# Kernel optimization log

Measured on AMD Instinct MI355X. Metric: run time of the kernel, lower is better.

Reference implementation:

```python
import jax, jax.numpy as jnp
import numpy as np

NUM_GRAPHS = 512
NODES_PER_GRAPH = 200  # == N_rois
EDGES_PER_GRAPH = 3200  # avg degree 16
N_ROIS = 200
HIDDEN = 64
OUT = 2


def setup_inputs() -> dict:
    key = jax.random.key(0)
    ks = jax.random.split(key, 7)
    N = NUM_GRAPHS * NODES_PER_GRAPH
    E = NUM_GRAPHS * EDGES_PER_GRAPH
    x = jax.random.normal(ks[0], (N, N_ROIS), dtype=jnp.float32)
    # edges sampled within each graph's node block
    base = jnp.repeat(jnp.arange(NUM_GRAPHS, dtype=jnp.int64) * NODES_PER_GRAPH, EDGES_PER_GRAPH)
    local = jax.random.randint(ks[1], (2, E), 0, NODES_PER_GRAPH, dtype=jnp.int64)
    edge_index = local + base[None, :]
    batch = jnp.arange(N, dtype=jnp.int64) // NODES_PER_GRAPH
    conv_w = jax.random.normal(ks[2], (N_ROIS, HIDDEN), dtype=jnp.float32) * 0.1
    conv_b = jax.random.normal(ks[3], (HIDDEN,), dtype=jnp.float32) * 0.1
    lin_w = jax.random.normal(ks[4], (HIDDEN, OUT), dtype=jnp.float32) * 0.1
    lin_b = jax.random.normal(ks[5], (OUT,), dtype=jnp.float32) * 0.1
    return {"x": x, "edge_index": edge_index, "batch": batch,
            "conv_w": conv_w, "conv_b": conv_b, "lin_w": lin_w, "lin_b": lin_b}


def reference(x, edge_index, batch, conv_w, conv_b, lin_w, lin_b):
    N = x.shape[0]
    # GCNConv: linear transform first (N_rois -> hidden), then normalized aggregation
    h = x @ conv_w  # [N, H]
    loops = jnp.arange(N, dtype=edge_index.dtype)
    src = jnp.concatenate([edge_index[0], loops])  # add self-loops (PyG default)
    dst = jnp.concatenate([edge_index[1], loops])
    deg = jax.ops.segment_sum(jnp.ones_like(dst, dtype=h.dtype), dst, num_segments=N)
    dinv = jnp.where(deg > 0, jax.lax.rsqrt(deg), jnp.zeros_like(deg))
    norm = dinv[src] * dinv[dst]  # D^-1/2 (A+I) D^-1/2 edge weights
    agg = jax.ops.segment_sum(h[src] * norm[:, None], dst, num_segments=N) + conv_b
    hr = jax.nn.relu(agg)
    x_pool = jax.ops.segment_max(hr, batch, num_segments=NUM_GRAPHS)  # [G, H]
    out = x_pool @ lin_w + lin_b  # [G, OUT]
    return out, x_pool
```

## Files before the change

kernel.cpp:

```cpp
#include <hip/hip_runtime.h>

#define NUM_GRAPHS 512
#define NPG 200
#define EPG 3200
#define NROIS 200
#define HID 64
#define OUTC 2
#define APITCH 232
#define HPITCH 232
#define XPITCH 72
#define WIMG_ELEMS (7 * 4 * 2 * 64 * 8)
#define WS_NEEDED ((size_t)WIMG_ELEMS * 2)

typedef short v8s __attribute__((ext_vector_type(8)));
typedef float v4f __attribute__((ext_vector_type(4)));

__device__ __forceinline__ unsigned bf16_rne(float f) {
  unsigned u = __float_as_uint(f);
  return (u + 0x7fffu + ((u >> 16) & 1u)) >> 16;
}

__global__ void prep_wimg(const float* __restrict__ cw, unsigned short* __restrict__ wimg) {
  int idx = blockIdx.x * 256 + threadIdx.x;
  if (idx >= WIMG_ELEMS) return;
  int i    = idx & 7;
  int lane = (idx >> 3) & 63;
  int hl   = (idx >> 9) & 1;
  int nt   = (idx >> 10) & 3;
  int kt   = idx >> 12;
  int k  = kt * 32 + (lane >> 4) * 8 + i;
  int ch = nt * 16 + (lane & 15);
  float f = (k < NROIS) ? cw[k * HID + ch] : 0.f;
  unsigned hi = bf16_rne(f);
  float lo = f - __uint_as_float(hi << 16);
  wimg[idx] = hl ? (unsigned short)(__float_as_uint(lo) >> 16) : (unsigned short)hi;
}

struct __align__(16) SmemU {
  union {
    struct {
      unsigned short xhi[NPG * XPITCH];
      unsigned short xlo[NPG * XPITCH];
    } g1;
    struct {
      unsigned char adj[208 * APITCH];
      unsigned short hpTl[HID * HPITCH];
    } g2;
  } u;
  float dinv[NPG];
  int cnt[NPG];
  int pool[HID];
};

__device__ __forceinline__ void stage_x(SmemU& s, const float* __restrict__ x,
                                        int base, int tk, int tid) {
  const int c0 = tk * 64;
  #pragma unroll
  for (int r = 0; r < 7; ++r) {
    int idx = tid + r * 512;
    if (idx < NPG * 16) {
      int node = idx >> 4;
      int f4 = idx & 15;
      int col = c0 + f4 * 4;
      float ff[4];
      if (col + 4 <= NROIS) {
        const float4 v = *(const float4*)(x + (size_t)(base + node) * NROIS + col);
        ff[0] = v.x; ff[1] = v.y; ff[2] = v.z; ff[3] = v.w;
      } else {
        #pragma unroll
        for (int e = 0; e < 4; ++e)
          ff[e] = (col + e < NROIS) ? x[(size_t)(base + node) * NROIS + col + e] : 0.f;
      }
      unsigned hh[4], ll[4];
      #pragma unroll
      for (int e = 0; e < 4; ++e) {
        unsigned uu = __float_as_uint(ff[e]);
        hh[e] = uu >> 16;
        float lo = ff[e] - __uint_as_float(hh[e] << 16);
        ll[e] = __float_as_uint(lo) >> 16;
      }
      uint2 ph = {hh[0] | (hh[1] << 16), hh[2] | (hh[3] << 16)};
      uint2 pl = {ll[0] | (ll[1] << 16), ll[2] | (ll[3] << 16)};
      *(uint2*)&s.u.g1.xhi[node * XPITCH + f4 * 4] = ph;
      *(uint2*)&s.u.g1.xlo[node * XPITCH + f4 * 4] = pl;
    }
  }
}

__global__ __launch_bounds__(512, 4)
void gcn_fused2(const float* __restrict__ x,
                const int* __restrict__ ei,
                const unsigned short* __restrict__ wimg,
                const float* __restrict__ cb,
                const float* __restrict__ lw,
                const float* __restrict__ lb,
                float* __restrict__ out,
                int Etot) {
  __shared__ SmemU s;
  const int g = blockIdx.x;
  const int tid = threadIdx.x;
  const int base = g * NPG;
  const int ebase = g * EPG;
  const int lane = tid & 63;
  const int w = __builtin_amdgcn_readfirstlane(tid >> 6);
  const int ml = tid & 15;
  const int q  = (tid >> 4) & 3;

  if (tid < NPG) s.cnt[tid] = 0;
  if (tid < HID) s.pool[tid] = 0;
  __syncthreads();

  int esrc[7], edst[7];
  #pragma unroll
  for (int r = 0; r < 7; ++r) {
    int e = tid + r * 512;
    esrc[r] = -1; edst[r] = 0;
    if (e < EPG) {
      esrc[r] = ei[ebase + e] - base;
      edst[r] = ei[Etot + ebase + e] - base;
      atomicAdd(&s.cnt[edst[r]], 1);
    }
  }
  stage_x(s, x, base, 0, tid);
  __syncthreads();

  if (tid < NPG) s.dinv[tid] = rsqrtf((float)(s.cnt[tid] + 1));

  int mts[2];
  mts[0] = w;
  mts[1] = (w < 5) ? 8 + w : -1;

  v4f acc[2][4];
  #pragma unroll
  for (int a = 0; a < 2; ++a)
    #pragma unroll
    for (int b = 0; b < 4; ++b)
      acc[a][b] = (v4f){0.f, 0.f, 0.f, 0.f};

  for (int tk = 0; tk < 4; ++tk) {
    #pragma unroll
    for (int half = 0; half < 2; ++half) {
      const int kt = tk * 2 + half;
      if (kt < 7) {
        const int koff = half * 32 + q * 8;
        v8s whi[4], wlo[4];
        #pragma unroll
        for (int nt = 0; nt < 4; ++nt) {
          const unsigned short* pw = wimg + (size_t)(((kt * 4 + nt) * 2) * 64 + lane) * 8;
          whi[nt] = *(const v8s*)pw;
          wlo[nt] = *(const v8s*)(pw + 64 * 8);
        }
        #pragma unroll
        for (int mi = 0; mi < 2; ++mi) {
          if (mts[mi] >= 0) {
            const int node = mts[mi] * 16 + ml;
            const int nrd = (node < NPG) ? node : 0;
            const v8s xh = *(const v8s*)&s.u.g1.xhi[nrd * XPITCH + koff];
            const v8s xl = *(const v8s*)&s.u.g1.xlo[nrd * XPITCH + koff];
            #pragma unroll
            for (int nt = 0; nt < 4; ++nt) {
              acc[mi][nt] = __builtin_amdgcn_mfma_f32_16x16x32_bf16(whi[nt], xl, acc[mi][nt], 0, 0, 0);
              acc[mi][nt] = __builtin_amdgcn_mfma_f32_16x16x32_bf16(wlo[nt], xh, acc[mi][nt], 0, 0, 0);
              acc[mi][nt] = __builtin_amdgcn_mfma_f32_16x16x32_bf16(whi[nt], xh, acc[mi][nt], 0, 0, 0);
            }
          }
        }
      }
    }
    __syncthreads();
    if (tk < 3) {
      stage_x(s, x, base, tk + 1, tid);
      __syncthreads();
    }
  }

  {
    uint4* z = (uint4*)&s.u;
    const uint4 z4 = {0u, 0u, 0u, 0u};
    #pragma unroll
    for (int i = 0; i < 10; ++i) {
      int idx = tid + i * 512;
      if (idx < (208 * APITCH + HID * HPITCH * 2) / 16) z[idx] = z4;
    }
  }
  __syncthreads();

  #pragma unroll
  for (int mi = 0; mi < 2; ++mi) {
    if (mts[mi] >= 0) {
      const int node = mts[mi] * 16 + ml;
      if (node < NPG) {
        const float dv = s.dinv[node];
        #pragma unroll
        for (int nt = 0; nt < 4; ++nt) {
          #pragma unroll
          for (int r = 0; r < 4; ++r) {
            const int ch = nt * 16 + q * 4 + r;
            s.u.g2.hpTl[ch * HPITCH + node] = (unsigned short)bf16_rne(dv * acc[mi][nt][r]);
          }
        }
      }
    }
  }
  {
    unsigned* adjW = (unsigned*)s.u.g2.adj;
    #pragma unroll
    for (int r = 0; r < 7; ++r) {
      if (esrc[r] >= 0) {
        int idx = edst[r] * APITCH + esrc[r];
        atomicAdd(&adjW[idx >> 2], 1u << ((idx & 3) * 8));
      }
    }
    if (tid < NPG) {
      int idx = tid * APITCH + tid;
      atomicAdd(&adjW[idx >> 2], 1u << ((idx & 3) * 8));
    }
  }
  __syncthreads();

  {
    v4f acc2[2][4];
    #pragma unroll
    for (int a = 0; a < 2; ++a)
      #pragma unroll
      for (int b = 0; b < 4; ++b)
        acc2[a][b] = (v4f){0.f, 0.f, 0.f, 0.f};

    for (int kt = 0; kt < 7; ++kt) {
      const int k0 = kt * 32 + q * 8;

      v8s bf[4];
      #pragma unroll
      for (int nt = 0; nt < 4; ++nt)
        bf[nt] = *(const v8s*)&s.u.g2.hpTl[(nt * 16 + ml) * HPITCH + k0];

      #pragma unroll
      for (int mi = 0; mi < 2; ++mi) {
        if (mts[mi] >= 0) {
          const int row = mts[mi] * 16 + ml;
          const uint2 dd = *(const uint2*)&s.u.g2.adj[row * APITCH + k0];
          v8s af;
          #pragma unroll
          for (int i = 0; i < 4; ++i) {
            af[i]     = (short)(__float_as_uint((float)((dd.x >> (8 * i)) & 0xffu)) >> 16);
            af[i + 4] = (short)(__float_as_uint((float)((dd.y >> (8 * i)) & 0xffu)) >> 16);
          }
          #pragma unroll
          for (int nt = 0; nt < 4; ++nt)
            acc2[mi][nt] = __builtin_amdgcn_mfma_f32_16x16x32_bf16(af, bf[nt], acc2[mi][nt], 0, 0, 0);
        }
      }
    }

    float cbv[4];
    #pragma unroll
    for (int nt = 0; nt < 4; ++nt) cbv[nt] = cb[nt * 16 + ml];
    float mx[4] = {0.f, 0.f, 0.f, 0.f};
    #pragma unroll
    for (int mi = 0; mi < 2; ++mi) {
      if (mts[mi] >= 0) {
        #pragma unroll
        for (int r = 0; r < 4; ++r) {
          const int row = mts[mi] * 16 + q * 4 + r;
          if (row < NPG) {
            const float dv = s.dinv[row];
            #pragma unroll
            for (int nt = 0; nt < 4; ++nt) {
              float v = fmaxf(fmaf(dv, acc2[mi][nt][r], cbv[nt]), 0.f);
              mx[nt] = fmaxf(mx[nt], v);
            }
          }
        }
      }
    }
    #pragma unroll
    for (int nt = 0; nt < 4; ++nt) {
      mx[nt] = fmaxf(mx[nt], __shfl_xor(mx[nt], 16));
      mx[nt] = fmaxf(mx[nt], __shfl_xor(mx[nt], 32));
    }
    if (q == 0 && (lane >> 5) == 0) {
      #pragma unroll
      for (int nt = 0; nt < 4; ++nt)
        atomicMax(&s.pool[nt * 16 + ml], __float_as_int(mx[nt]));
    }
  }
  __syncthreads();

  if (tid < HID) {
    const float xp = __int_as_float(s.pool[tid]);
    out[NUM_GRAPHS * OUTC + g * HID + tid] = xp;
    float p0 = xp * lw[tid * 2 + 0];
    float p1 = xp * lw[tid * 2 + 1];
    #pragma unroll
    for (int off = 32; off > 0; off >>= 1) {
      p0 += __shfl_down(p0, off);
      p1 += __shfl_down(p1, off);
    }
    if (tid == 0) {
      out[g * OUTC + 0] = p0 + lb[0];
      out[g * OUTC + 1] = p1 + lb[1];
    }
  }
}

struct __align__(16) SmemF {
  unsigned char adj[208 * APITCH];
  unsigned short hpT[HID * HPITCH];
  float dinv[NPG];
  int cnt[NPG];
  int pool[HID];
};

__global__ __launch_bounds__(512, 4)
void gcn_fused_fb(const float* __restrict__ x,
                  const int* __restrict__ ei,
                  const float* __restrict__ cw,
                  const float* __restrict__ cb,
                  const float* __restrict__ lw,
                  const float* __restrict__ lb,
                  float* __restrict__ out,
                  int Etot) {
  __shared__ SmemF s;
  const int g = blockIdx.x;
  const int tid = threadIdx.x;
  const int base = g * NPG;
  const int ebase = g * EPG;
  const int lane = tid & 63;
  const int w = __builtin_amdgcn_readfirstlane(tid >> 6);
  const int ml = tid & 15;
  const int q  = (tid >> 4) & 3;

  {
    uint4* z = (uint4*)&s;
    const uint4 z4 = {0u, 0u, 0u, 0u};
    #pragma unroll
    for (int i = 0; i < 10; ++i) {
      int idx = tid + i * 512;
      if (idx < (208 * APITCH + HID * HPITCH * 2) / 16) z[idx] = z4;
    }
    if (tid < NPG) s.cnt[tid] = 0;
    if (tid < HID) s.pool[tid] = 0;
  }
  __syncthreads();

  int esrc[7], edst[7];
  #pragma unroll
  for (int r = 0; r < 7; ++r) {
    int e = tid + r * 512;
    esrc[r] = -1; edst[r] = 0;
    if (e < EPG) {
      esrc[r] = ei[ebase + e] - base;
      edst[r] = ei[Etot + ebase + e] - base;
      atomicAdd(&s.cnt[edst[r]], 1);
    }
  }
  __syncthreads();

  if (tid < NPG) s.dinv[tid] = rsqrtf((float)(s.cnt[tid] + 1));

  {
    unsigned* adjW = (unsigned*)s.adj;
    #pragma unroll
    for (int r = 0; r < 7; ++r) {
      if (esrc[r] >= 0) {
        int idx = edst[r] * APITCH + esrc[r];
        atomicAdd(&adjW[idx >> 2], 1u << ((idx & 3) * 8));
      }
    }
    if (tid < NPG) {
      int idx = tid * APITCH + tid;
      atomicAdd(&adjW[idx >> 2], 1u << ((idx & 3) * 8));
    }
  }
  __syncthreads();

  {
    int mts[2];
    mts[0] = w;
    mts[1] = (w < 5) ? 8 + w : -1;
    v4f acc[2][4];
    #pragma unroll
    for (int a = 0; a < 2; ++a)
      #pragma unroll
      for (int b = 0; b < 4; ++b)
        acc[a][b] = (v4f){0.f, 0.f, 0.f, 0.f};

    for (int kt = 0; kt < 7; ++kt) {
      const int k0 = kt * 32 + q * 8;
      const bool kok = (k0 < NROIS);
      v8s bhi[4], blo[4];
      #pragma unroll
      for (int nt = 0; nt < 4; ++nt) {
        #pragma unroll
        for (int i = 0; i < 8; ++i) {
          float f = kok ? cw[(k0 + i) * HID + nt * 16 + ml] : 0.f;
          unsigned hb = bf16_rne(f);
          float lo = f - __uint_as_float(hb << 16);
          bhi[nt][i] = (short)hb;
          blo[nt][i] = (short)(__float_as_uint(lo) >> 16);
        }
      }
      #pragma unroll
      for (int mi = 0; mi < 2; ++mi) {
        if (mts[mi] >= 0) {
          const int row = mts[mi] * 16 + ml;
          v8s ahi, alo;
          if (kok && row < NPG) {
            const float* px = x + (size_t)(base + row) * NROIS + k0;
            const float4 f0 = *(const float4*)px;
            const float4 f1 = *(const float4*)(px + 4);
            const float ff[8] = {f0.x, f0.y, f0.z, f0.w, f1.x, f1.y, f1.z, f1.w};
            #pragma unroll
            for (int i = 0; i < 8; ++i) {
              unsigned u = __float_as_uint(ff[i]);
              unsigned hb = u >> 16;
              float lo = ff[i] - __uint_as_float(hb << 16);
              ahi[i] = (short)hb;
              alo[i] = (short)(__float_as_uint(lo) >> 16);
            }
          } else {
            #pragma unroll
            for (int i = 0; i < 8; ++i) { ahi[i] = 0; alo[i] = 0; }
          }
          #pragma unroll
          for (int nt = 0; nt < 4; ++nt) {
            acc[mi][nt] = __builtin_amdgcn_mfma_f32_16x16x32_bf16(ahi, blo[nt], acc[mi][nt], 0, 0, 0);
            acc[mi][nt] = __builtin_amdgcn_mfma_f32_16x16x32_bf16(alo, bhi[nt], acc[mi][nt], 0, 0, 0);
            acc[mi][nt] = __builtin_amdgcn_mfma_f32_16x16x32_bf16(ahi, bhi[nt], acc[mi][nt], 0, 0, 0);
          }
        }
      }
    }
    #pragma unroll
    for (int mi = 0; mi < 2; ++mi) {
      if (mts[mi] >= 0) {
        #pragma unroll
        for (int r = 0; r < 4; ++r) {
          const int row = mts[mi] * 16 + q * 4 + r;
          if (row < NPG) {
            const float dv = s.dinv[row];
            #pragma unroll
            for (int nt = 0; nt < 4; ++nt)
              s.hpT[(nt * 16 + ml) * HPITCH + row] =
                  (unsigned short)bf16_rne(dv * acc[mi][nt][r]);
          }
        }
      }
    }
  }
  __syncthreads();

  {
    int mts[2];
    mts[0] = w;
    mts[1] = (w < 5) ? 8 + w : -1;
    v4f acc2[2][4];
    #pragma unroll
    for (int a = 0; a < 2; ++a)
      #pragma unroll
      for (int b = 0; b < 4; ++b)
        acc2[a][b] = (v4f){0.f, 0.f, 0.f, 0.f};

    for (int kt = 0; kt < 7; ++kt) {
      const int k0 = kt * 32 + q * 8;
      v8s bf[4];
      #pragma unroll
      for (int nt = 0; nt < 4; ++nt)
        bf[nt] = *(const v8s*)&s.hpT[(nt * 16 + ml) * HPITCH + k0];
      #pragma unroll
      for (int mi = 0; mi < 2; ++mi) {
        if (mts[mi] >= 0) {
          const int row = mts[mi] * 16 + ml;
          const uint2 dd = *(const uint2*)&s.adj[row * APITCH + k0];
          v8s af;
          #pragma unroll
          for (int i = 0; i < 4; ++i) {
            af[i]     = (short)(__float_as_uint((float)((dd.x >> (8 * i)) & 0xffu)) >> 16);
            af[i + 4] = (short)(__float_as_uint((float)((dd.y >> (8 * i)) & 0xffu)) >> 16);
          }
          #pragma unroll
          for (int nt = 0; nt < 4; ++nt)
            acc2[mi][nt] = __builtin_amdgcn_mfma_f32_16x16x32_bf16(af, bf[nt], acc2[mi][nt], 0, 0, 0);
        }
      }
    }

    float cbv[4];
    #pragma unroll
    for (int nt = 0; nt < 4; ++nt) cbv[nt] = cb[nt * 16 + ml];
    float mx[4] = {0.f, 0.f, 0.f, 0.f};
    #pragma unroll
    for (int mi = 0; mi < 2; ++mi) {
      if (mts[mi] >= 0) {
        #pragma unroll
        for (int r = 0; r < 4; ++r) {
          const int row = mts[mi] * 16 + q * 4 + r;
          if (row < NPG) {
            const float dv = s.dinv[row];
            #pragma unroll
            for (int nt = 0; nt < 4; ++nt) {
              float v = fmaxf(fmaf(dv, acc2[mi][nt][r], cbv[nt]), 0.f);
              mx[nt] = fmaxf(mx[nt], v);
            }
          }
        }
      }
    }
    #pragma unroll
    for (int nt = 0; nt < 4; ++nt) {
      mx[nt] = fmaxf(mx[nt], __shfl_xor(mx[nt], 16));
      mx[nt] = fmaxf(mx[nt], __shfl_xor(mx[nt], 32));
    }
    if (q == 0 && (lane >> 5) == 0) {
      #pragma unroll
      for (int nt = 0; nt < 4; ++nt)
        atomicMax(&s.pool[nt * 16 + ml], __float_as_int(mx[nt]));
    }
  }
  __syncthreads();

  if (tid < HID) {
    const float xp = __int_as_float(s.pool[tid]);
    out[NUM_GRAPHS * OUTC + g * HID + tid] = xp;
    float p0 = xp * lw[tid * 2 + 0];
    float p1 = xp * lw[tid * 2 + 1];
    #pragma unroll
    for (int off = 32; off > 0; off >>= 1) {
      p0 += __shfl_down(p0, off);
      p1 += __shfl_down(p1, off);
    }
    if (tid == 0) {
      out[g * OUTC + 0] = p0 + lb[0];
      out[g * OUTC + 1] = p1 + lb[1];
    }
  }
}

extern "C" void kernel_launch(void* const* d_in, const int* in_sizes, int n_in,
                              void* d_out, int out_size, void* d_ws, size_t ws_size,
                              hipStream_t stream) {
  const float* x  = (const float*)d_in[0];
  const int*   ei = (const int*)d_in[1];
  const float* cw = (const float*)d_in[3];
  const float* cb = (const float*)d_in[4];
  const float* lw = (const float*)d_in[5];
  const float* lb = (const float*)d_in[6];
  const int Etot = in_sizes[1] / 2;

  if (ws_size >= WS_NEEDED) {
    unsigned short* wimg = (unsigned short*)d_ws;
    prep_wimg<<<(WIMG_ELEMS + 255) / 256, 256, 0, stream>>>(cw, wimg);
    gcn_fused2<<<NUM_GRAPHS, 512, 0, stream>>>(x, ei, wimg, cb, lw, lb,
                                               (float*)d_out, Etot);
  } else {
    gcn_fused_fb<<<NUM_GRAPHS, 512, 0, stream>>>(x, ei, cw, cb, lw, lb,
                                                 (float*)d_out, Etot);
  }
}
```

Before: 154.5 us.

## Register-prefetch x tiles, build adjacency early, derive degree from adjacency rows

The x staging is split into a global load into registers and a later shared-memory write. The next 32-column tile is now prefetched while MFMAs run on the current one, so global latency overlaps compute. The adjacency matrix moves out of the union and is built at kernel start, which removes the separate count atomics. Degrees are then computed by summing byte counts in each adjacency row. This adds more barriers (seven k-steps instead of four), more registers for the prefetch, and a different shared-memory footprint that may affect occupancy.

```diff
diff --git a/kernel.cpp b/kernel.cpp
--- a/kernel.cpp
+++ b/kernel.cpp
@@ -8,7 +8,7 @@
 #define OUTC 2
 #define APITCH 232
 #define HPITCH 232
-#define XPITCH 72
+#define XPITCH 40
 #define WIMG_ELEMS (7 * 4 * 2 * 64 * 8)
 #define WS_NEEDED ((size_t)WIMG_ELEMS * 2)
 
@@ -37,40 +37,37 @@
 }
 
 struct __align__(16) SmemU {
+  unsigned char adj[208 * APITCH];
   union {
-    struct {
-      unsigned short xhi[NPG * XPITCH];
-      unsigned short xlo[NPG * XPITCH];
-    } g1;
-    struct {
-      unsigned char adj[208 * APITCH];
-      unsigned short hpTl[HID * HPITCH];
-    } g2;
+    struct { unsigned short xhi[NPG * XPITCH];
+             unsigned short xlo[NPG * XPITCH]; } g1;
+    unsigned short hpTl[HID * HPITCH];
   } u;
   float dinv[NPG];
-  int cnt[NPG];
   int pool[HID];
 };
 
-__device__ __forceinline__ void stage_x(SmemU& s, const float* __restrict__ x,
-                                        int base, int tk, int tid) {
-  const int c0 = tk * 64;
+__device__ __forceinline__ void xload(float4* xf, const float* __restrict__ x,
+                                      int base, int c0, int tid) {
   #pragma unroll
-  for (int r = 0; r < 7; ++r) {
+  for (int r = 0; r < 4; ++r) {
     int idx = tid + r * 512;
-    if (idx < NPG * 16) {
-      int node = idx >> 4;
-      int f4 = idx & 15;
-      int col = c0 + f4 * 4;
-      float ff[4];
-      if (col + 4 <= NROIS) {
-        const float4 v = *(const float4*)(x + (size_t)(base + node) * NROIS + col);
-        ff[0] = v.x; ff[1] = v.y; ff[2] = v.z; ff[3] = v.w;
-      } else {
-        #pragma unroll
-        for (int e = 0; e < 4; ++e)
-          ff[e] = (col + e < NROIS) ? x[(size_t)(base + node) * NROIS + col + e] : 0.f;
-      }
+    int node = idx >> 3, f4 = idx & 7;
+    int col = c0 + f4 * 4;
+    if (idx < 1600 && col + 4 <= NROIS)
+      xf[r] = *(const float4*)(x + (size_t)(base + node) * NROIS + col);
+    else
+      xf[r] = make_float4(0.f, 0.f, 0.f, 0.f);
+  }
+}
+
+__device__ __forceinline__ void xwrite(SmemU& s, const float4* xf, int tid) {
+  #pragma unroll
+  for (int r = 0; r < 4; ++r) {
+    int idx = tid + r * 512;
+    if (idx < 1600) {
+      int node = idx >> 3, f4 = idx & 7;
+      const float ff[4] = {xf[r].x, xf[r].y, xf[r].z, xf[r].w};
       unsigned hh[4], ll[4];
       #pragma unroll
       for (int e = 0; e < 4; ++e) {
@@ -88,7 +85,7 @@
 }
 
 __global__ __launch_bounds__(512, 4)
-void gcn_fused2(const float* __restrict__ x,
+void gcn_fused3(const float* __restrict__ x,
                 const int* __restrict__ ei,
                 const unsigned short* __restrict__ wimg,
                 const float* __restrict__ cb,
@@ -106,10 +103,8 @@
   const int ml = tid & 15;
   const int q  = (tid >> 4) & 3;
 
-  if (tid < NPG) s.cnt[tid] = 0;
-  if (tid < HID) s.pool[tid] = 0;
-  __syncthreads();
-
+  float4 xf[4];
+  xload(xf, x, base, 0, tid);
   int esrc[7], edst[7];
   #pragma unroll
   for (int r = 0; r < 7; ++r) {
@@ -118,13 +113,36 @@
     if (e < EPG) {
       esrc[r] = ei[ebase + e] - base;
       edst[r] = ei[Etot + ebase + e] - base;
-      atomicAdd(&s.cnt[edst[r]], 1);
-    }
-  }
-  stage_x(s, x, base, 0, tid);
-  __syncthreads();
-
-  if (tid < NPG) s.dinv[tid] = rsqrtf((float)(s.cnt[tid] + 1));
+    }
+  }
+  {
+    uint4* z = (uint4*)s.adj;
+    const uint4 z4 = {0u, 0u, 0u, 0u};
+    #pragma unroll
+    for (int i = 0; i < 6; ++i) {
+      int idx = tid + i * 512;
+      if (idx < (208 * APITCH) / 16) z[idx] = z4;
+    }
+    if (tid < HID) s.pool[tid] = 0;
+  }
+  __syncthreads();
+
+  {
+    unsigned* adjW = (unsigned*)s.adj;
+    #pragma unroll
+    for (int r = 0; r < 7; ++r) {
+      if (esrc[r] >= 0) {
+        int idx = edst[r] * APITCH + esrc[r];
+        atomicAdd(&adjW[idx >> 2], 1u << ((idx & 3) * 8));
+      }
+    }
+    if (tid < NPG) {
+      int idx = tid * APITCH + tid;
+      atomicAdd(&adjW[idx >> 2], 1u << ((idx & 3) * 8));
+    }
+  }
+  xwrite(s, xf, tid);
+  __syncthreads();
 
   int mts[2];
   mts[0] = w;
@@ -137,51 +155,50 @@
     for (int b = 0; b < 4; ++b)
       acc[a][b] = (v4f){0.f, 0.f, 0.f, 0.f};
 
-  for (int tk = 0; tk < 4; ++tk) {
-    #pragma unroll
-    for (int half = 0; half < 2; ++half) {
-      const int kt = tk * 2 + half;
-      if (kt < 7) {
-        const int koff = half * 32 + q * 8;
-        v8s whi[4], wlo[4];
+  for (int kt = 0; kt < 7; ++kt) {
+    float4 xfn[4];
+    if (kt < 6) xload(xfn, x, base, (kt + 1) * 32, tid);
+
+    v8s whi[4], wlo[4];
+    #pragma unroll
+    for (int nt = 0; nt < 4; ++nt) {
+      const unsigned short* pw = wimg + (size_t)(((kt * 4 + nt) * 2) * 64 + lane) * 8;
+      whi[nt] = *(const v8s*)pw;
+      wlo[nt] = *(const v8s*)(pw + 64 * 8);
+    }
+    #pragma unroll
+    for (int mi = 0; mi < 2; ++mi) {
+      if (mts[mi] >= 0) {
+        const int node = mts[mi] * 16 + ml;
+        const int nrd = (node < NPG) ? node : 0;
+        const v8s xh = *(const v8s*)&s.u.g1.xhi[nrd * XPITCH + q * 8];
+        const v8s xl = *(const v8s*)&s.u.g1.xlo[nrd * XPITCH + q * 8];
         #pragma unroll
         for (int nt = 0; nt < 4; ++nt) {
-          const unsigned short* pw = wimg + (size_t)(((kt * 4 + nt) * 2) * 64 + lane) * 8;
-          whi[nt] = *(const v8s*)pw;
-          wlo[nt] = *(const v8s*)(pw + 64 * 8);
-        }
-        #pragma unroll
-        for (int mi = 0; mi < 2; ++mi) {
-          if (mts[mi] >= 0) {
-            const int node = mts[mi] * 16 + ml;
-            const int nrd = (node < NPG) ? node : 0;
-            const v8s xh = *(const v8s*)&s.u.g1.xhi[nrd * XPITCH + koff];
-            const v8s xl = *(const v8s*)&s.u.g1.xlo[nrd * XPITCH + koff];
-            #pragma unroll
-            for (int nt = 0; nt < 4; ++nt) {
-              acc[mi][nt] = __builtin_amdgcn_mfma_f32_16x16x32_bf16(whi[nt], xl, acc[mi][nt], 0, 0, 0);
-              acc[mi][nt] = __builtin_amdgcn_mfma_f32_16x16x32_bf16(wlo[nt], xh, acc[mi][nt], 0, 0, 0);
-              acc[mi][nt] = __builtin_amdgcn_mfma_f32_16x16x32_bf16(whi[nt], xh, acc[mi][nt], 0, 0, 0);
-            }
-          }
+          acc[mi][nt] = __builtin_amdgcn_mfma_f32_16x16x32_bf16(whi[nt], xl, acc[mi][nt], 0, 0, 0);
+          acc[mi][nt] = __builtin_amdgcn_mfma_f32_16x16x32_bf16(wlo[nt], xh, acc[mi][nt], 0, 0, 0);
+          acc[mi][nt] = __builtin_amdgcn_mfma_f32_16x16x32_bf16(whi[nt], xh, acc[mi][nt], 0, 0, 0);
         }
       }
     }
     __syncthreads();
-    if (tk < 3) {
-      stage_x(s, x, base, tk + 1, tid);
+    if (kt < 6) {
+      xwrite(s, xfn, tid);
       __syncthreads();
     }
   }
 
-  {
-    uint4* z = (uint4*)&s.u;
-    const uint4 z4 = {0u, 0u, 0u, 0u};
-    #pragma unroll
-    for (int i = 0; i < 10; ++i) {
-      int idx = tid + i * 512;
-      if (idx < (208 * APITCH + HID * HPITCH * 2) / 16) z[idx] = z4;
-    }
+  if (tid < NPG) {
+    const unsigned* ap = (const unsigned*)s.adj + tid * (APITCH / 4);
+    unsigned ssum = 0;
+    #pragma unroll 2
+    for (int j = 0; j < APITCH / 4; ++j)
+      ssum += (ap[j] * 0x01010101u) >> 24;
+    s.dinv[tid] = rsqrtf((float)ssum);
+  }
+  {
+    int ch = tid >> 3, grp = tid & 7;
+    *(uint2*)&s.u.hpTl[ch * HPITCH + 200 + grp * 4] = (uint2){0u, 0u};
   }
   __syncthreads();
 
@@ -196,24 +213,10 @@
           #pragma unroll
           for (int r = 0; r < 4; ++r) {
             const int ch = nt * 16 + q * 4 + r;
-            s.u.g2.hpTl[ch * HPITCH + node] = (unsigned short)bf16_rne(dv * acc[mi][nt][r]);
-          }
-        }
-      }
-    }
-  }
-  {
-    unsigned* adjW = (unsigned*)s.u.g2.adj;
-    #pragma unroll
-    for (int r = 0; r < 7; ++r) {
-      if (esrc[r] >= 0) {
-        int idx = edst[r] * APITCH + esrc[r];
-        atomicAdd(&adjW[idx >> 2], 1u << ((idx & 3) * 8));
-      }
-    }
-    if (tid < NPG) {
-      int idx = tid * APITCH + tid;
-      atomicAdd(&adjW[idx >> 2], 1u << ((idx & 3) * 8));
+            s.u.hpTl[ch * HPITCH + node] = (unsigned short)bf16_rne(dv * acc[mi][nt][r]);
+          }
+        }
+      }
     }
   }
   __syncthreads();
@@ -232,13 +235,13 @@
       v8s bf[4];
       #pragma unroll
       for (int nt = 0; nt < 4; ++nt)
-        bf[nt] = *(const v8s*)&s.u.g2.hpTl[(nt * 16 + ml) * HPITCH + k0];
+        bf[nt] = *(const v8s*)&s.u.hpTl[(nt * 16 + ml) * HPITCH + k0];
 
       #pragma unroll
       for (int mi = 0; mi < 2; ++mi) {
         if (mts[mi] >= 0) {
           const int row = mts[mi] * 16 + ml;
-          const uint2 dd = *(const uint2*)&s.u.g2.adj[row * APITCH + k0];
+          const uint2 dd = *(const uint2*)&s.adj[row * APITCH + k0];
           v8s af;
           #pragma unroll
           for (int i = 0; i < 4; ++i) {
@@ -550,7 +553,7 @@
   if (ws_size >= WS_NEEDED) {
     unsigned short* wimg = (unsigned short*)d_ws;
     prep_wimg<<<(WIMG_ELEMS + 255) / 256, 256, 0, stream>>>(cw, wimg);
-    gcn_fused2<<<NUM_GRAPHS, 512, 0, stream>>>(x, ei, wimg, cb, lw, lb,
+    gcn_fused3<<<NUM_GRAPHS, 512, 0, stream>>>(x, ei, wimg, cb, lw, lb,
                                                (float*)d_out, Etot);
   } else {
     gcn_fused_fb<<<NUM_GRAPHS, 512, 0, stream>>>(x, ei, cw, cb, lw, lb,
```

After: 151.4 us. 2.0% less time.
